# Optimization experiments

Hardware: AMD Instinct MI355X
Metric: run time of the kernel (lower is better)

The kernel has to match this reference:

```python
import jax, jax.numpy as jnp
import numpy as np

B, C, P, NG, NCLS, HID, N, IMG = 2, 256, 7, 2, 81, 1024, 512, 800
STRIDES = [4, 8, 16, 32]
SCALE = 56.0  # roi_map_level_scale


def _roi_align(feat, rois, pooled, scale, ng):
    """torchvision-legacy (aligned=False) ROI Align. feat [B,C,H,W], rois [N,5]."""
    Bf, Cf, H, W = feat.shape
    ft = jnp.transpose(feat, (0, 2, 3, 1))  # [B,H,W,C]
    b = rois[:, 0].astype(jnp.int32)
    x1, y1, x2, y2 = (rois[:, i] * scale for i in (1, 2, 3, 4))
    rw = jnp.maximum(x2 - x1, 1.0)
    rh = jnp.maximum(y2 - y1, 1.0)
    # sample grid per output bin: ng points per axis, centered in sub-bins
    g = (jnp.arange(pooled)[:, None] + (jnp.arange(ng)[None, :] + 0.5) / ng).reshape(-1)  # [P*ng]
    ys = y1[:, None] + g[None, :] * (rh / pooled)[:, None]  # [N,S]
    xs = x1[:, None] + g[None, :] * (rw / pooled)[:, None]

    def axis(coord, size):
        valid = (coord >= -1.0) & (coord <= size)
        c = jnp.clip(coord, 0.0, size - 1)
        lo = jnp.floor(c).astype(jnp.int32)
        hi = jnp.minimum(lo + 1, size - 1)
        return valid, lo, hi, c - lo

    vy, ylo, yhi, fy = axis(ys, H)
    vx, xlo, xhi, fx = axis(xs, W)
    bb = b[:, None, None]

    def gather(yi, xi):
        return ft[bb, yi[:, :, None], xi[:, None, :], :]  # [N,S,S,C]

    wy = fy[:, :, None, None]
    wx = fx[:, None, :, None]
    val = ((1 - wy) * (1 - wx) * gather(ylo, xlo) + (1 - wy) * wx * gather(ylo, xhi)
           + wy * (1 - wx) * gather(yhi, xlo) + wy * wx * gather(yhi, xhi))
    val = jnp.where((vy[:, :, None] & vx[:, None, :])[..., None], val, 0.0)
    val = val.reshape(-1, pooled, ng, pooled, ng, Cf).mean(axis=(2, 4))  # [N,P,P,C]
    return jnp.transpose(val, (0, 3, 1, 2))  # [N,C,P,P]


def setup_inputs() -> dict:
    key = jax.random.key(0)
    ks = jax.random.split(key, 16)
    feats = {}
    for i, s in enumerate(STRIDES):
        hw = IMG // s
        feats[f"p{i+2}"] = jax.random.normal(ks[i], (B, C, hw, hw), jnp.float32)
    # realistic proposals: batch idx + boxes with sizes 16..512 px
    bidx = jax.random.randint(ks[4], (N,), 0, B).astype(jnp.float32)
    sw = 2.0 ** jax.random.uniform(ks[5], (N,), minval=4.0, maxval=9.0)
    sh = 2.0 ** jax.random.uniform(ks[6], (N,), minval=4.0, maxval=9.0)
    x1 = jax.random.uniform(ks[7], (N,)) * (IMG - sw)
    y1 = jax.random.uniform(ks[8], (N,)) * (IMG - sh)
    rois = jnp.stack([bidx, x1, y1, x1 + sw - 1, y1 + sh - 1], axis=1)
    D = C * P * P
    inp = dict(feats, rois=rois,
               w1=0.01 * jax.random.normal(ks[9], (HID, D), jnp.float32),
               b1=jnp.zeros((HID,), jnp.float32),
               w2=0.01 * jax.random.normal(ks[10], (HID, HID), jnp.float32),
               b2=jnp.zeros((HID,), jnp.float32),
               w_cls=0.01 * jax.random.normal(ks[11], (NCLS, HID), jnp.float32),
               b_cls=jnp.zeros((NCLS,), jnp.float32),
               w_reg=0.001 * jax.random.normal(ks[12], (NCLS * 4, HID), jnp.float32),
               b_reg=jnp.zeros((NCLS * 4,), jnp.float32))
    return inp


def reference(p2, p3, p4, p5, rois, w1, b1, w2, b2, w_cls, b_cls, w_reg, b_reg):
    feats = [p2, p3, p4, p5]
    # FPN level assignment (same math as torch: log2(sqrt(hw)/scale + 1e-6), floor, clamp)
    rh = rois[:, 4] - rois[:, 2] + 1
    rw = rois[:, 3] - rois[:, 1] + 1
    levels = jnp.clip(jnp.floor(jnp.log2(jnp.sqrt(rh * rw) / SCALE + 1e-6)), 0, 3).astype(jnp.int32)
    # dispatch: compute each ROI on its assigned level (masked combine == gather/sort-scatter)
    pooled = jnp.zeros((rois.shape[0], C, P, P), rois.dtype)
    for l, feat in enumerate(feats):
        pl = _roi_align(feat, rois, P, 1.0 / STRIDES[l], NG)
        pooled = pooled + jnp.where((levels == l)[:, None, None, None], pl, 0.0)
    x = pooled.reshape(pooled.shape[0], -1)  # [N, C*P*P]
    x = jax.nn.relu(x @ w1.T + b1)
    x = jax.nn.relu(x @ w2.T + b2)
    x_cls = x @ w_cls.T + b_cls
    x_reg = x @ w_reg.T + b_reg  # TEST mode, not class-agnostic: no gather
    cls_probs = jax.nn.softmax(x_cls, axis=1)
    rois_out = rois.reshape(B, -1, 5)
    cls_probs = cls_probs.reshape(B, rois_out.shape[1], -1)
    bbox_preds = x_reg.reshape(B, rois_out.shape[1], -1)
    return rois_out, cls_probs, bbox_preds
```

## Files before the change

### kernel.cpp

```cpp
#include <hip/hip_runtime.h>
#include <hip/hip_bf16.h>
#include <math.h>

#define NROI   512
#define CCH    256
#define POOLP  7
#define DDIM   12544
#define HIDN   1024
#define NCLS   81
#define NREG   324
#define NHEAD  512
#define OUT_ROIS   2560
#define OUT_CLS    (512*81)

typedef __attribute__((ext_vector_type(4))) float f32x4;
typedef __attribute__((ext_vector_type(8))) short bf16x8;

static __device__ __forceinline__ unsigned short f2bf(float x) {
    __hip_bfloat16 h = __float2bfloat16(x);
    return *reinterpret_cast<unsigned short*>(&h);
}
static __device__ __forceinline__ float bf2f(unsigned short u) {
    unsigned int b = ((unsigned int)u) << 16;
    return *reinterpret_cast<float*>(&b);
}

#define PS_B0 10
#define PS_B1 (PS_B0 + 768)
#define PS_B2 (PS_B1 + 1024)
#define PS_B3 (PS_B2 + 1024)
__global__ __launch_bounds__(256) void prep_small_k(const float* __restrict__ rois,
                                                    const float* __restrict__ w2,
                                                    const float* __restrict__ wc,
                                                    const float* __restrict__ wr,
                                                    float* __restrict__ out,
                                                    float* __restrict__ accz,
                                                    unsigned short* __restrict__ w2b,
                                                    unsigned short* __restrict__ whd) {
    int bid = blockIdx.x, t = threadIdx.x;
    if (bid < PS_B0) {
        int i = bid * 256 + t;
        if (i < OUT_ROIS) out[i] = rois[i];
    } else if (bid < PS_B1) {
        int i = (bid - PS_B0) * 256 + t;
        ((float4*)accz)[i] = make_float4(0.f, 0.f, 0.f, 0.f);
    } else if (bid < PS_B2) {
        int i = (bid - PS_B1) * 256 + t;
        float4 v = ((const float4*)w2)[i];
        ushort4 o;
        o.x = f2bf(v.x); o.y = f2bf(v.y); o.z = f2bf(v.z); o.w = f2bf(v.w);
        ((ushort4*)w2b)[i] = o;
    } else {
        int i2 = (bid - PS_B2) * 256 + t;
        int r = i2 >> 9, c = (i2 & 511) << 1;
        float v0, v1;
        if (r < NCLS)             { v0 = wc[r * HIDN + c]; v1 = wc[r * HIDN + c + 1]; }
        else if (r < NCLS + NREG) { v0 = wr[(r - NCLS) * HIDN + c]; v1 = wr[(r - NCLS) * HIDN + c + 1]; }
        else                      { v0 = 0.f; v1 = 0.f; }
        ((unsigned int*)whd)[i2] = (unsigned int)f2bf(v0) | ((unsigned int)f2bf(v1) << 16);
    }
}

__global__ __launch_bounds__(256) void permute_w1_k(const float* __restrict__ w1,
                                                    unsigned short* __restrict__ w1b) {
    __shared__ unsigned short lw[49 * 258];
    int n = blockIdx.x, t = threadIdx.x;
    const float* src = w1 + (size_t)n * DDIM;
    for (int k = t; k < DDIM; k += 256) {
        int c = k / 49;
        int s = k - c * 49;
        lw[s * 258 + c] = f2bf(src[k]);
    }
    __syncthreads();
    unsigned int* dst = (unsigned int*)(w1b + (size_t)n * DDIM);
    for (int j2 = t; j2 < DDIM / 2; j2 += 256) {
        int s = j2 >> 7, c2 = (j2 & 127) << 1;
        dst[j2] = lw[s * 258 + c2] | ((unsigned int)lw[s * 258 + c2 + 1] << 16);
    }
}

__global__ __launch_bounds__(256) void transpose_k(const float* __restrict__ p2,
                                                   const float* __restrict__ p3,
                                                   const float* __restrict__ p4,
                                                   const float* __restrict__ p5,
                                                   unsigned short* __restrict__ f0,
                                                   unsigned short* __restrict__ f1,
                                                   unsigned short* __restrict__ f2,
                                                   unsigned short* __restrict__ f3) {
    __shared__ unsigned short sm[64][264];
    int idx = blockIdx.x;
    const float* in; unsigned short* op; int S, nS, base;
    if (idx < 1250)      { in = p2; op = f0; S = 40000; nS = 625; base = 0; }
    else if (idx < 1564) { in = p3; op = f1; S = 10000; nS = 157; base = 1250; }
    else if (idx < 1644) { in = p4; op = f2; S = 2500;  nS = 40;  base = 1564; }
    else                 { in = p5; op = f3; S = 625;   nS = 10;  base = 1644; }
    int j  = idx - base;
    int b  = j / nS;
    int s0 = (j - b * nS) * 64;
    int t  = threadIdx.x;

    int k = t & 15, g = t >> 4;
    bool vec = (s0 + 64 <= S);
    const float* src0 = in + ((size_t)(b * CCH + g * 16)) * S + s0 + k * 4;
#pragma unroll
    for (int jj = 0; jj < 16; jj++) {
        const float* src = src0 + (size_t)jj * S;
        int c = g * 16 + jj;
        if (vec) {
            float4 v = *(const float4*)src;
            sm[k * 4 + 0][c] = f2bf(v.x); sm[k * 4 + 1][c] = f2bf(v.y);
            sm[k * 4 + 2][c] = f2bf(v.z); sm[k * 4 + 3][c] = f2bf(v.w);
        } else {
#pragma unroll
            for (int e = 0; e < 4; e++)
                sm[k * 4 + e][c] = (s0 + k * 4 + e < S) ? f2bf(src[e]) : (unsigned short)0;
        }
    }
    __syncthreads();

    int L = t & 63, w = t >> 6;
#pragma unroll
    for (int i = 0; i < 16; i++) {
        int s = w * 16 + i;
        if (s0 + s < S) {
            ushort4 u = *(const ushort4*)&sm[s][4 * L];
            uint2 v;
            v.x = (unsigned int)u.x | ((unsigned int)u.y << 16);
            v.y = (unsigned int)u.z | ((unsigned int)u.w << 16);
            *(uint2*)(op + ((size_t)b * S + s0 + s) * CCH + 4 * L) = v;
        }
    }
}

__global__ __launch_bounds__(256) void roi_align_k(const unsigned short* __restrict__ f0,
                                                   const unsigned short* __restrict__ f1,
                                                   const unsigned short* __restrict__ f2,
                                                   const unsigned short* __restrict__ f3,
                                                   const float* __restrict__ rois,
                                                   unsigned short* __restrict__ xpool) {
    __shared__ float s_f[16];
    __shared__ int   s_lo[16], s_hi[16], s_v[16];

    int py = blockIdx.x, r = blockIdx.y, t = threadIdx.x;

    float r0  = rois[r * 5 + 0];
    float rx1 = rois[r * 5 + 1], ry1 = rois[r * 5 + 2];
    float rx2 = rois[r * 5 + 3], ry2 = rois[r * 5 + 4];
    int b = (int)r0;

    float aw = rx2 - rx1 + 1.f, ah = ry2 - ry1 + 1.f;
    float lvf = floorf(log2f(sqrtf(ah * aw) / 56.f + 1e-6f));
    int lv = (int)fminf(fmaxf(lvf, 0.f), 3.f);

    const unsigned short* F = (lv == 0) ? f0 : (lv == 1) ? f1 : (lv == 2) ? f2 : f3;
    int HW      = (lv == 0) ? 200 : (lv == 1) ? 100 : (lv == 2) ? 50 : 25;
    float scale = (lv == 0) ? 0.25f : (lv == 1) ? 0.125f : (lv == 2) ? 0.0625f : 0.03125f;

    float x1 = rx1 * scale, yy1 = ry1 * scale;
    float x2 = rx2 * scale, yy2 = ry2 * scale;
    float rw = fmaxf(x2 - x1, 1.f), rh = fmaxf(yy2 - yy1, 1.f);

    if (t < 16) {
        bool isY = t < 2;
        float coord;
        if (isY) {
            float g = (float)py + ((float)t + 0.5f) * 0.5f;
            coord = yy1 + g * (rh * (1.f / 7.f));
        } else {
            int j = t - 2;
            float g = (float)(j >> 1) + ((float)(j & 1) + 0.5f) * 0.5f;
            coord = x1 + g * (rw * (1.f / 7.f));
        }
        int vld = (coord >= -1.f && coord <= (float)HW) ? 1 : 0;
        float c = fminf(fmaxf(coord, 0.f), (float)(HW - 1));
        int lo  = (int)floorf(c);
        int hi  = min(lo + 1, HW - 1);
        s_v[t] = vld; s_lo[t] = lo; s_hi[t] = hi; s_f[t] = c - (float)lo;
    }
    __syncthreads();

    const unsigned short* Fb = F + ((size_t)b * HW * HW) * CCH + t;
    size_t obase = (size_t)r * DDIM + py * 7 * 256 + t;

    for (int px = 0; px < POOLP; px++) {
        float acc = 0.f;
#pragma unroll
        for (int s = 0; s < 4; s++) {
            int iy = s >> 1;
            int ix = px * 2 + (s & 1);
            int vy = s_v[iy], vx = s_v[2 + ix];
            if (vy & vx) {
                float fy = s_f[iy], fx = s_f[2 + ix];
                int ylo = s_lo[iy], yhi = s_hi[iy];
                int xlo = s_lo[2 + ix], xhi = s_hi[2 + ix];
                float v00 = bf2f(Fb[((size_t)ylo * HW + xlo) * CCH]);
                float v01 = bf2f(Fb[((size_t)ylo * HW + xhi) * CCH]);
                float v10 = bf2f(Fb[((size_t)yhi * HW + xlo) * CCH]);
                float v11 = bf2f(Fb[((size_t)yhi * HW + xhi) * CCH]);
                acc += (1.f - fy) * ((1.f - fx) * v00 + fx * v01)
                     + fy * ((1.f - fx) * v10 + fx * v11);
            }
        }
        xpool[obase + px * 256] = f2bf(acc * 0.25f);
    }
}

__global__ __launch_bounds__(256) void roi_align_nchw_k(const float* __restrict__ f0,
                                                        const float* __restrict__ f1,
                                                        const float* __restrict__ f2,
                                                        const float* __restrict__ f3,
                                                        const float* __restrict__ rois,
                                                        unsigned short* __restrict__ xpool) {
    __shared__ float s_f[16];
    __shared__ int   s_lo[16], s_hi[16], s_v[16];
    int py = blockIdx.x, r = blockIdx.y, t = threadIdx.x;
    float r0  = rois[r * 5 + 0];
    float rx1 = rois[r * 5 + 1], ry1 = rois[r * 5 + 2];
    float rx2 = rois[r * 5 + 3], ry2 = rois[r * 5 + 4];
    int b = (int)r0;
    float aw = rx2 - rx1 + 1.f, ah = ry2 - ry1 + 1.f;
    float lvf = floorf(log2f(sqrtf(ah * aw) / 56.f + 1e-6f));
    int lv = (int)fminf(fmaxf(lvf, 0.f), 3.f);
    const float* F = (lv == 0) ? f0 : (lv == 1) ? f1 : (lv == 2) ? f2 : f3;
    int HW      = (lv == 0) ? 200 : (lv == 1) ? 100 : (lv == 2) ? 50 : 25;
    float scale = (lv == 0) ? 0.25f : (lv == 1) ? 0.125f : (lv == 2) ? 0.0625f : 0.03125f;
    float x1 = rx1 * scale, yy1 = ry1 * scale;
    float x2 = rx2 * scale, yy2 = ry2 * scale;
    float rw = fmaxf(x2 - x1, 1.f), rh = fmaxf(yy2 - yy1, 1.f);
    if (t < 16) {
        bool isY = t < 2;
        float coord;
        if (isY) {
            float g = (float)py + ((float)t + 0.5f) * 0.5f;
            coord = yy1 + g * (rh * (1.f / 7.f));
        } else {
            int j = t - 2;
            float g = (float)(j >> 1) + ((float)(j & 1) + 0.5f) * 0.5f;
            coord = x1 + g * (rw * (1.f / 7.f));
        }
        int vld = (coord >= -1.f && coord <= (float)HW) ? 1 : 0;
        float c = fminf(fmaxf(coord, 0.f), (float)(HW - 1));
        int lo  = (int)floorf(c);
        int hi  = min(lo + 1, HW - 1);
        s_v[t] = vld; s_lo[t] = lo; s_hi[t] = hi; s_f[t] = c - (float)lo;
    }
    __syncthreads();
    const float* Fb = F + ((size_t)b * CCH + t) * HW * HW;
    size_t obase = (size_t)r * DDIM + py * 7 * 256 + t;
    for (int px = 0; px < POOLP; px++) {
        float acc = 0.f;
#pragma unroll
        for (int s = 0; s < 4; s++) {
            int iy = s >> 1, ix = px * 2 + (s & 1);
            int vy = s_v[iy], vx = s_v[2 + ix];
            if (vy & vx) {
                float fy = s_f[iy], fx = s_f[2 + ix];
                int ylo = s_lo[iy], yhi = s_hi[iy];
                int xlo = s_lo[2 + ix], xhi = s_hi[2 + ix];
                float v00 = Fb[(size_t)ylo * HW + xlo];
                float v01 = Fb[(size_t)ylo * HW + xhi];
                float v10 = Fb[(size_t)yhi * HW + xlo];
                float v11 = Fb[(size_t)yhi * HW + xhi];
                acc += (1.f - fy) * ((1.f - fx) * v00 + fx * v01)
                     + fy * ((1.f - fx) * v10 + fx * v11);
            }
        }
        xpool[obase + px * 256] = f2bf(acc * 0.25f);
    }
}

__global__ __launch_bounds__(256) void gemm_bf16_k(const unsigned short* __restrict__ A,
                                                   const unsigned short* __restrict__ W,
                                                   float* __restrict__ Cacc,
                                                   int M, int N, int K, int kchunk) {
    __shared__ __align__(16) unsigned short As[2][8][64][8];
    __shared__ __align__(16) unsigned short Ws[2][8][64][8];

    int t = threadIdx.x;
    int lane = t & 63, wid = t >> 6;
    int m0 = blockIdx.y * 64, n0 = blockIdx.x * 64;
    int k0 = blockIdx.z * kchunk;
    int wm = (wid >> 1) * 32, wn = (wid & 1) * 32;
    int fr = lane & 15, kg = lane >> 4;
    int nsteps = kchunk >> 6;

    f32x4 acc[2][2] = {};

    const unsigned short* Arow = A + (size_t)(m0 + lane) * K;
    const unsigned short* Wrow = W + (size_t)(n0 + lane) * K;

    auto stage = [&](int buf, int kb) {
#pragma unroll
        for (int i = 0; i < 2; i++) {
            int c = wid * 2 + i;
            __builtin_amdgcn_global_load_lds(
                (const __attribute__((address_space(1))) void*)(Arow + kb + c * 8),
                (__attribute__((address_space(3))) void*)(&As[buf][c][0][0]), 16, 0, 0);
            __builtin_amdgcn_global_load_lds(
                (const __attribute__((address_space(1))) void*)(Wrow + kb + c * 8),
                (__attribute__((address_space(3))) void*)(&Ws[buf][c][0][0]), 16, 0, 0);
        }
    };

    stage(0, k0);
    __syncthreads();
    int cur = 0;
    for (int tt = 0; tt < nsteps; ++tt) {
        if (tt + 1 < nsteps) stage(cur ^ 1, k0 + (tt + 1) * 64);
#pragma unroll
        for (int h = 0; h < 2; h++) {
            bf16x8 a0 = *(const bf16x8*)(&As[cur][h * 4 + kg][wm + fr][0]);
            bf16x8 a1 = *(const bf16x8*)(&As[cur][h * 4 + kg][wm + 16 + fr][0]);
            bf16x8 b0 = *(const bf16x8*)(&Ws[cur][h * 4 + kg][wn + fr][0]);
            bf16x8 b1 = *(const bf16x8*)(&Ws[cur][h * 4 + kg][wn + 16 + fr][0]);
            acc[0][0] = __builtin_amdgcn_mfma_f32_16x16x32_bf16(a0, b0, acc[0][0], 0, 0, 0);
            acc[0][1] = __builtin_amdgcn_mfma_f32_16x16x32_bf16(a0, b1, acc[0][1], 0, 0, 0);
            acc[1][0] = __builtin_amdgcn_mfma_f32_16x16x32_bf16(a1, b0, acc[1][0], 0, 0, 0);
            acc[1][1] = __builtin_amdgcn_mfma_f32_16x16x32_bf16(a1, b1, acc[1][1], 0, 0, 0);
        }
        __syncthreads();
        cur ^= 1;
    }

    int row = m0 + wm + (lane >> 4) * 4;
    int col = n0 + wn + fr;
#pragma unroll
    for (int fm = 0; fm < 2; fm++)
#pragma unroll
        for (int fn = 0; fn < 2; fn++)
#pragma unroll
            for (int r = 0; r < 4; r++)
                atomicAdd(&Cacc[(size_t)(row + fm * 16 + r) * N + col + fn * 16],
                          acc[fm][fn][r]);
}

__global__ __launch_bounds__(256) void gemm128_bf16_k(const unsigned short* __restrict__ A,
                                                      const unsigned short* __restrict__ W,
                                                      float* __restrict__ Cp,
                                                      int M, int N, int K, int kchunk) {
    __shared__ __align__(16) unsigned short As[2][8][64][8];
    __shared__ __align__(16) unsigned short Ws[2][8][128][8];

    int lin  = blockIdx.x;
    int nb   = (lin & 7) * 112 + (lin >> 3);
    int tile = nb / 14, bz = nb - tile * 14;
    int bx = tile >> 3, by = tile & 7;

    int t = threadIdx.x;
    int lane = t & 63, wid = t >> 6;
    int m0 = by * 64, n0 = bx * 128;
    int k0 = bz * kchunk;
    int wm = (wid >> 1) * 32, wn = (wid & 1) * 64;
    int fr = lane & 15, kg = lane >> 4;
    int nsteps = kchunk >> 6;

    f32x4 acc[2][4] = {};

    const unsigned short* Arow = A + (size_t)(m0 + lane) * K;

    auto stage = [&](int buf, int kb) {
#pragma unroll
        for (int i = 0; i < 6; i++) {
            int c = wid * 6 + i;
            if (c < 8) {
                __builtin_amdgcn_global_load_lds(
                    (const __attribute__((address_space(1))) void*)(Arow + kb + c * 8),
                    (__attribute__((address_space(3))) void*)(&As[buf][c][0][0]), 16, 0, 0);
            } else {
                int idx = c - 8, kgc = idx & 7, rh = idx >> 3;
                __builtin_amdgcn_global_load_lds(
                    (const __attribute__((address_space(1))) void*)
                        (W + (size_t)(n0 + rh * 64 + lane) * K + kb + kgc * 8),
                    (__attribute__((address_space(3))) void*)(&Ws[buf][kgc][rh * 64][0]),
                    16, 0, 0);
            }
        }
    };

    stage(0, k0);
    __syncthreads();
    int cur = 0;
    for (int tt = 0; tt < nsteps; ++tt) {
        if (tt + 1 < nsteps) stage(cur ^ 1, k0 + (tt + 1) * 64);
#pragma unroll
        for (int h = 0; h < 2; h++) {
            bf16x8 av[2], bv[4];
#pragma unroll
            for (int f = 0; f < 2; f++)
                av[f] = *(const bf16x8*)(&As[cur][h * 4 + kg][wm + f * 16 + fr][0]);
#pragma unroll
            for (int f = 0; f < 4; f++)
                bv[f] = *(const bf16x8*)(&Ws[cur][h * 4 + kg][wn + f * 16 + fr][0]);
#pragma unroll
            for (int fm = 0; fm < 2; fm++)
#pragma unroll
                for (int fn = 0; fn < 4; fn++)
                    acc[fm][fn] = __builtin_amdgcn_mfma_f32_16x16x32_bf16(
                        av[fm], bv[fn], acc[fm][fn], 0, 0, 0);
        }
        __syncthreads();
        cur ^= 1;
    }

    float* Cout = Cp + (size_t)bz * ((size_t)M * N);
    int row = m0 + wm + (lane >> 4) * 4;
    int col = n0 + wn + fr;
#pragma unroll
    for (int fm = 0; fm < 2; fm++)
#pragma unroll
        for (int fn = 0; fn < 4; fn++)
#pragma unroll
            for (int r = 0; r < 4; r++)
                Cout[(size_t)(row + fm * 16 + r) * N + col + fn * 16] = acc[fm][fn][r];
}

__global__ __launch_bounds__(256) void fc_ep_k(const float* __restrict__ Cp,
                                               const float* __restrict__ bias,
                                               unsigned short* __restrict__ dst,
                                               int MN, int ks) {
    int i = blockIdx.x * 256 + threadIdx.x;
    if (i >= MN) return;
    float s = 0.f;
    for (int p = 0; p < ks; p++) s += Cp[(size_t)p * MN + i];
    s = fmaxf(s + bias[i & (HIDN - 1)], 0.f);
    dst[i] = f2bf(s);
}

__global__ void head_ep_k(const float* __restrict__ hf,
                          const float* __restrict__ bc,
                          const float* __restrict__ br,
                          float* __restrict__ out) {
    int r = blockIdx.x, l = threadIdx.x;
    const float* row = hf + (size_t)r * NHEAD;

    float* reg = out + OUT_ROIS + OUT_CLS + (size_t)r * NREG;
    for (int j = l; j < NREG; j += 64) reg[j] = row[NCLS + j] + br[j];

    float v0 = row[l] + bc[l];
    float v1 = (l + 64 < NCLS) ? row[l + 64] + bc[l + 64] : -INFINITY;
    float m = fmaxf(v0, v1);
#pragma unroll
    for (int o = 32; o; o >>= 1) m = fmaxf(m, __shfl_xor(m, o));
    float e0 = __expf(v0 - m);
    float e1 = (l + 64 < NCLS) ? __expf(v1 - m) : 0.f;
    float s = e0 + e1;
#pragma unroll
    for (int o = 32; o; o >>= 1) s += __shfl_xor(s, o);
    float inv = 1.f / s;
    float* cls = out + OUT_ROIS + (size_t)r * NCLS;
    cls[l] = e0 * inv;
    if (l + 64 < NCLS) cls[l + 64] = e1 * inv;
}

extern "C" void kernel_launch(void* const* d_in, const int* in_sizes, int n_in,
                              void* d_out, int out_size, void* d_ws, size_t ws_size,
                              hipStream_t stream) {
    const float* p2   = (const float*)d_in[0];
    const float* p3   = (const float*)d_in[1];
    const float* p4   = (const float*)d_in[2];
    const float* p5   = (const float*)d_in[3];
    const float* rois = (const float*)d_in[4];
    const float* w1   = (const float*)d_in[5];
    const float* b1   = (const float*)d_in[6];
    const float* w2   = (const float*)d_in[7];
    const float* b2   = (const float*)d_in[8];
    const float* wc   = (const float*)d_in[9];
    const float* bc   = (const float*)d_in[10];
    const float* wr   = (const float*)d_in[11];
    const float* br   = (const float*)d_in[12];

    float* out = (float*)d_out;

    const int KS1 = 14;

    char* p = (char*)d_ws;
    auto alloc = [&](size_t bytes) { char* r = p; p += (bytes + 255) & ~(size_t)255; return r; };
    unsigned short* xpool = (unsigned short*)alloc((size_t)NROI * DDIM * 2);
    unsigned short* y1b   = (unsigned short*)alloc((size_t)NROI * HIDN * 2);
    unsigned short* y2b   = (unsigned short*)alloc((size_t)NROI * HIDN * 2);
    unsigned short* w1b   = (unsigned short*)alloc((size_t)HIDN * DDIM * 2);
    unsigned short* w2b   = (unsigned short*)alloc((size_t)HIDN * HIDN * 2);
    unsigned short* whd   = (unsigned short*)alloc((size_t)NHEAD * HIDN * 2);
    float*          accz  = (float*)alloc((size_t)(NROI * HIDN + NROI * NHEAD) * 4);
    unsigned short* ft0 = (unsigned short*)alloc((size_t)2 * 40000 * CCH * 2);
    unsigned short* ft1 = (unsigned short*)alloc((size_t)2 * 10000 * CCH * 2);
    unsigned short* ft2 = (unsigned short*)alloc((size_t)2 * 2500 * CCH * 2);
    unsigned short* ft3 = (unsigned short*)alloc((size_t)2 * 625 * CCH * 2);
    bool nhwc = (size_t)(p - (char*)d_ws) <= ws_size;

    float* y2f = accz;
    float* hf  = accz + (size_t)NROI * HIDN;
    float* part = (float*)ft0;

    prep_small_k<<<PS_B3, 256, 0, stream>>>(rois, w2, wc, wr, out, accz, w2b, whd);
    permute_w1_k<<<HIDN, 256, 0, stream>>>(w1, w1b);

    if (nhwc) {
        transpose_k<<<1664, 256, 0, stream>>>(p2, p3, p4, p5, ft0, ft1, ft2, ft3);
        roi_align_k<<<dim3(POOLP, NROI), 256, 0, stream>>>(ft0, ft1, ft2, ft3, rois, xpool);
    } else {
        roi_align_nchw_k<<<dim3(POOLP, NROI), 256, 0, stream>>>(p2, p3, p4, p5, rois, xpool);
    }

    gemm128_bf16_k<<<8 * 8 * KS1, 256, 0, stream>>>(
        xpool, w1b, part, NROI, HIDN, DDIM, DDIM / KS1);
    fc_ep_k<<<(NROI * HIDN + 255) / 256, 256, 0, stream>>>(part, b1, y1b, NROI * HIDN, KS1);

    gemm_bf16_k<<<dim3(HIDN / 64, NROI / 64, 2), 256, 0, stream>>>(
        y1b, w2b, y2f, NROI, HIDN, HIDN, HIDN / 2);
    fc_ep_k<<<(NROI * HIDN + 255) / 256, 256, 0, stream>>>(y2f, b2, y2b, NROI * HIDN, 1);

    gemm_bf16_k<<<dim3(NHEAD / 64, NROI / 64, 4), 256, 0, stream>>>(
        y2b, whd, hf, NROI, NHEAD, HIDN, HIDN / 4);
    head_ep_k<<<NROI, 64, 0, stream>>>(hf, bc, br, out);
}
```

Measured before the change: 185.1 us.

## Merge weight prep kernels, retile feature transpose, fuse FC2 epilogue into GEMM

Three changes at once. The w1 permute is folded into the small prep kernel, removing one launch. The NCHW-to-NHWC transpose now uses 128-spatial by 64-channel tiles with an XOR-swizzled LDS layout in place of padding. The second FC GEMM drops its split-K atomics, the zeroing of its accumulator and the separate epilogue kernel, and applies bias plus ReLU directly while writing bf16. The cost is that FC2 now runs on only 128 blocks with no K split, which lowers parallelism, and the transpose's LDS reads become scalar 2-byte accesses.

```diff
diff --git a/kernel.cpp b/kernel.cpp
--- a/kernel.cpp
+++ b/kernel.cpp
@@ -26,31 +26,35 @@
 }
 
 #define PS_B0 10
-#define PS_B1 (PS_B0 + 768)
+#define PS_B1 (PS_B0 + 256)
 #define PS_B2 (PS_B1 + 1024)
 #define PS_B3 (PS_B2 + 1024)
-__global__ __launch_bounds__(256) void prep_small_k(const float* __restrict__ rois,
-                                                    const float* __restrict__ w2,
-                                                    const float* __restrict__ wc,
-                                                    const float* __restrict__ wr,
-                                                    float* __restrict__ out,
-                                                    float* __restrict__ accz,
-                                                    unsigned short* __restrict__ w2b,
-                                                    unsigned short* __restrict__ whd) {
+#define PS_B4 (PS_B3 + 1024)
+__global__ __launch_bounds__(256) void prep_k(const float* __restrict__ rois,
+                                              const float* __restrict__ w1,
+                                              const float* __restrict__ w2,
+                                              const float* __restrict__ wc,
+                                              const float* __restrict__ wr,
+                                              float* __restrict__ out,
+                                              float* __restrict__ hf,
+                                              unsigned short* __restrict__ w1b,
+                                              unsigned short* __restrict__ w2b,
+                                              unsigned short* __restrict__ whd) {
+    __shared__ unsigned short lw[49 * 258];
     int bid = blockIdx.x, t = threadIdx.x;
     if (bid < PS_B0) {
         int i = bid * 256 + t;
         if (i < OUT_ROIS) out[i] = rois[i];
     } else if (bid < PS_B1) {
         int i = (bid - PS_B0) * 256 + t;
-        ((float4*)accz)[i] = make_float4(0.f, 0.f, 0.f, 0.f);
+        ((float4*)hf)[i] = make_float4(0.f, 0.f, 0.f, 0.f);
     } else if (bid < PS_B2) {
         int i = (bid - PS_B1) * 256 + t;
         float4 v = ((const float4*)w2)[i];
         ushort4 o;
         o.x = f2bf(v.x); o.y = f2bf(v.y); o.z = f2bf(v.z); o.w = f2bf(v.w);
         ((ushort4*)w2b)[i] = o;
-    } else {
+    } else if (bid < PS_B3) {
         int i2 = (bid - PS_B2) * 256 + t;
         int r = i2 >> 9, c = (i2 & 511) << 1;
         float v0, v1;
@@ -58,24 +62,20 @@
         else if (r < NCLS + NREG) { v0 = wr[(r - NCLS) * HIDN + c]; v1 = wr[(r - NCLS) * HIDN + c + 1]; }
         else                      { v0 = 0.f; v1 = 0.f; }
         ((unsigned int*)whd)[i2] = (unsigned int)f2bf(v0) | ((unsigned int)f2bf(v1) << 16);
-    }
-}
-
-__global__ __launch_bounds__(256) void permute_w1_k(const float* __restrict__ w1,
-                                                    unsigned short* __restrict__ w1b) {
-    __shared__ unsigned short lw[49 * 258];
-    int n = blockIdx.x, t = threadIdx.x;
-    const float* src = w1 + (size_t)n * DDIM;
-    for (int k = t; k < DDIM; k += 256) {
-        int c = k / 49;
-        int s = k - c * 49;
-        lw[s * 258 + c] = f2bf(src[k]);
-    }
-    __syncthreads();
-    unsigned int* dst = (unsigned int*)(w1b + (size_t)n * DDIM);
-    for (int j2 = t; j2 < DDIM / 2; j2 += 256) {
-        int s = j2 >> 7, c2 = (j2 & 127) << 1;
-        dst[j2] = lw[s * 258 + c2] | ((unsigned int)lw[s * 258 + c2 + 1] << 16);
+    } else {
+        int n = bid - PS_B3;
+        const float* src = w1 + (size_t)n * DDIM;
+        for (int k = t; k < DDIM; k += 256) {
+            int c = k / 49;
+            int s = k - c * 49;
+            lw[s * 258 + c] = f2bf(src[k]);
+        }
+        __syncthreads();
+        unsigned int* dst = (unsigned int*)(w1b + (size_t)n * DDIM);
+        for (int j2 = t; j2 < DDIM / 2; j2 += 256) {
+            int s = j2 >> 7, c2 = (j2 & 127) << 1;
+            dst[j2] = lw[s * 258 + c2] | ((unsigned int)lw[s * 258 + c2 + 1] << 16);
+        }
     }
 }
 
@@ -87,47 +87,58 @@
                                                    unsigned short* __restrict__ f1,
                                                    unsigned short* __restrict__ f2,
                                                    unsigned short* __restrict__ f3) {
-    __shared__ unsigned short sm[64][264];
+    __shared__ unsigned short sm[128][66];
     int idx = blockIdx.x;
-    const float* in; unsigned short* op; int S, nS, base;
-    if (idx < 1250)      { in = p2; op = f0; S = 40000; nS = 625; base = 0; }
-    else if (idx < 1564) { in = p3; op = f1; S = 10000; nS = 157; base = 1250; }
-    else if (idx < 1644) { in = p4; op = f2; S = 2500;  nS = 40;  base = 1564; }
-    else                 { in = p5; op = f3; S = 625;   nS = 10;  base = 1644; }
-    int j  = idx - base;
-    int b  = j / nS;
-    int s0 = (j - b * nS) * 64;
+    const float* in; unsigned short* op; int S, base;
+    if (idx < 313)      { in = p2; op = f0; S = 40000; base = 0; }
+    else if (idx < 392) { in = p3; op = f1; S = 10000; base = 313; }
+    else if (idx < 412) { in = p4; op = f2; S = 2500;  base = 392; }
+    else                { in = p5; op = f3; S = 625;   base = 412; }
+    int s0 = (idx - base) * 128;
+    int c0 = blockIdx.y * 64;
+    int b  = blockIdx.z;
     int t  = threadIdx.x;
 
-    int k = t & 15, g = t >> 4;
-    bool vec = (s0 + 64 <= S);
-    const float* src0 = in + ((size_t)(b * CCH + g * 16)) * S + s0 + k * 4;
-#pragma unroll
-    for (int jj = 0; jj < 16; jj++) {
-        const float* src = src0 + (size_t)jj * S;
-        int c = g * 16 + jj;
+    int k = t & 31, g = t >> 5;
+    bool vec = (s0 + 128 <= S);
+#pragma unroll
+    for (int jj = 0; jj < 8; jj++) {
+        int c = g + jj * 8;
+        const float* src = in + ((size_t)(b * CCH + c0 + c)) * S + s0 + k * 4;
         if (vec) {
             float4 v = *(const float4*)src;
-            sm[k * 4 + 0][c] = f2bf(v.x); sm[k * 4 + 1][c] = f2bf(v.y);
-            sm[k * 4 + 2][c] = f2bf(v.z); sm[k * 4 + 3][c] = f2bf(v.w);
+#pragma unroll
+            for (int e = 0; e < 4; e++) {
+                int s = k * 4 + e;
+                float val = (e == 0) ? v.x : (e == 1) ? v.y : (e == 2) ? v.z : v.w;
+                sm[s][c ^ ((s & 7) << 3)] = f2bf(val);
+            }
         } else {
 #pragma unroll
-            for (int e = 0; e < 4; e++)
-                sm[k * 4 + e][c] = (s0 + k * 4 + e < S) ? f2bf(src[e]) : (unsigned short)0;
+            for (int e = 0; e < 4; e++) {
+                int s = k * 4 + e;
+                sm[s][c ^ ((s & 7) << 3)] =
+                    (s0 + s < S) ? f2bf(src[e]) : (unsigned short)0;
+            }
         }
     }
     __syncthreads();
 
-    int L = t & 63, w = t >> 6;
-#pragma unroll
-    for (int i = 0; i < 16; i++) {
-        int s = w * 16 + i;
+    int lane = t & 63, w = t >> 6;
+    int rl = lane >> 4, cw = (lane & 15) * 4;
+#pragma unroll
+    for (int i = 0; i < 8; i++) {
+        int s = w * 32 + i * 4 + rl;
         if (s0 + s < S) {
-            ushort4 u = *(const ushort4*)&sm[s][4 * L];
+            int sw = (s & 7) << 3;
+            unsigned short u0 = sm[s][(cw + 0) ^ sw];
+            unsigned short u1 = sm[s][(cw + 1) ^ sw];
+            unsigned short u2 = sm[s][(cw + 2) ^ sw];
+            unsigned short u3 = sm[s][(cw + 3) ^ sw];
             uint2 v;
-            v.x = (unsigned int)u.x | ((unsigned int)u.y << 16);
-            v.y = (unsigned int)u.z | ((unsigned int)u.w << 16);
-            *(uint2*)(op + ((size_t)b * S + s0 + s) * CCH + 4 * L) = v;
+            v.x = (unsigned int)u0 | ((unsigned int)u1 << 16);
+            v.y = (unsigned int)u2 | ((unsigned int)u3 << 16);
+            *(uint2*)(op + ((size_t)b * S + s0 + s) * CCH + c0 + cw) = v;
         }
     }
 }
@@ -334,6 +345,74 @@
                           acc[fm][fn][r]);
 }
 
+__global__ __launch_bounds__(256) void gemm_fc2_k(const unsigned short* __restrict__ A,
+                                                  const unsigned short* __restrict__ W,
+                                                  const float* __restrict__ bias,
+                                                  unsigned short* __restrict__ dst,
+                                                  int M, int N, int K) {
+    __shared__ __align__(16) unsigned short As[2][8][64][8];
+    __shared__ __align__(16) unsigned short Ws[2][8][64][8];
+
+    int t = threadIdx.x;
+    int lane = t & 63, wid = t >> 6;
+    int m0 = blockIdx.y * 64, n0 = blockIdx.x * 64;
+    int wm = (wid >> 1) * 32, wn = (wid & 1) * 32;
+    int fr = lane & 15, kg = lane >> 4;
+    int nsteps = K >> 6;
+
+    f32x4 acc[2][2] = {};
+
+    const unsigned short* Arow = A + (size_t)(m0 + lane) * K;
+    const unsigned short* Wrow = W + (size_t)(n0 + lane) * K;
+
+    auto stage = [&](int buf, int kb) {
+#pragma unroll
+        for (int i = 0; i < 2; i++) {
+            int c = wid * 2 + i;
+            __builtin_amdgcn_global_load_lds(
+                (const __attribute__((address_space(1))) void*)(Arow + kb + c * 8),
+                (__attribute__((address_space(3))) void*)(&As[buf][c][0][0]), 16, 0, 0);
+            __builtin_amdgcn_global_load_lds(
+                (const __attribute__((address_space(1))) void*)(Wrow + kb + c * 8),
+                (__attribute__((address_space(3))) void*)(&Ws[buf][c][0][0]), 16, 0, 0);
+        }
+    };
+
+    stage(0, 0);
+    __syncthreads();
+    int cur = 0;
+    for (int tt = 0; tt < nsteps; ++tt) {
+        if (tt + 1 < nsteps) stage(cur ^ 1, (tt + 1) * 64);
+#pragma unroll
+        for (int h = 0; h < 2; h++) {
+            bf16x8 a0 = *(const bf16x8*)(&As[cur][h * 4 + kg][wm + fr][0]);
+            bf16x8 a1 = *(const bf16x8*)(&As[cur][h * 4 + kg][wm + 16 + fr][0]);
+            bf16x8 b0 = *(const bf16x8*)(&Ws[cur][h * 4 + kg][wn + fr][0]);
+            bf16x8 b1 = *(const bf16x8*)(&Ws[cur][h * 4 + kg][wn + 16 + fr][0]);
+            acc[0][0] = __builtin_amdgcn_mfma_f32_16x16x32_bf16(a0, b0, acc[0][0], 0, 0, 0);
+            acc[0][1] = __builtin_amdgcn_mfma_f32_16x16x32_bf16(a0, b1, acc[0][1], 0, 0, 0);
+            acc[1][0] = __builtin_amdgcn_mfma_f32_16x16x32_bf16(a1, b0, acc[1][0], 0, 0, 0);
+            acc[1][1] = __builtin_amdgcn_mfma_f32_16x16x32_bf16(a1, b1, acc[1][1], 0, 0, 0);
+        }
+        __syncthreads();
+        cur ^= 1;
+    }
+
+    int row = m0 + wm + (lane >> 4) * 4;
+    int col = n0 + wn + fr;
+#pragma unroll
+    for (int fm = 0; fm < 2; fm++)
+#pragma unroll
+        for (int fn = 0; fn < 2; fn++) {
+            float bv = bias[col + fn * 16];
+#pragma unroll
+            for (int r = 0; r < 4; r++) {
+                float v = fmaxf(acc[fm][fn][r] + bv, 0.f);
+                dst[(size_t)(row + fm * 16 + r) * N + col + fn * 16] = f2bf(v);
+            }
+        }
+}
+
 __global__ __launch_bounds__(256) void gemm128_bf16_k(const unsigned short* __restrict__ A,
                                                       const unsigned short* __restrict__ W,
                                                       float* __restrict__ Cp,
@@ -481,22 +560,20 @@
     unsigned short* w1b   = (unsigned short*)alloc((size_t)HIDN * DDIM * 2);
     unsigned short* w2b   = (unsigned short*)alloc((size_t)HIDN * HIDN * 2);
     unsigned short* whd   = (unsigned short*)alloc((size_t)NHEAD * HIDN * 2);
-    float*          accz  = (float*)alloc((size_t)(NROI * HIDN + NROI * NHEAD) * 4);
+    float*          hf    = (float*)alloc((size_t)NROI * NHEAD * 4);
     unsigned short* ft0 = (unsigned short*)alloc((size_t)2 * 40000 * CCH * 2);
     unsigned short* ft1 = (unsigned short*)alloc((size_t)2 * 10000 * CCH * 2);
     unsigned short* ft2 = (unsigned short*)alloc((size_t)2 * 2500 * CCH * 2);
     unsigned short* ft3 = (unsigned short*)alloc((size_t)2 * 625 * CCH * 2);
     bool nhwc = (size_t)(p - (char*)d_ws) <= ws_size;
 
-    float* y2f = accz;
-    float* hf  = accz + (size_t)NROI * HIDN;
     float* part = (float*)ft0;
 
-    prep_small_k<<<PS_B3, 256, 0, stream>>>(rois, w2, wc, wr, out, accz, w2b, whd);
-    permute_w1_k<<<HIDN, 256, 0, stream>>>(w1, w1b);
+    prep_k<<<PS_B4, 256, 0, stream>>>(rois, w1, w2, wc, wr, out, hf, w1b, w2b, whd);
 
     if (nhwc) {
-        transpose_k<<<1664, 256, 0, stream>>>(p2, p3, p4, p5, ft0, ft1, ft2, ft3);
+        transpose_k<<<dim3(417, 4, 2), 256, 0, stream>>>(p2, p3, p4, p5,
+                                                         ft0, ft1, ft2, ft3);
         roi_align_k<<<dim3(POOLP, NROI), 256, 0, stream>>>(ft0, ft1, ft2, ft3, rois, xpool);
     } else {
         roi_align_nchw_k<<<dim3(POOLP, NROI), 256, 0, stream>>>(p2, p3, p4, p5, rois, xpool);
@@ -506,9 +583,8 @@
         xpool, w1b, part, NROI, HIDN, DDIM, DDIM / KS1);
     fc_ep_k<<<(NROI * HIDN + 255) / 256, 256, 0, stream>>>(part, b1, y1b, NROI * HIDN, KS1);
 
-    gemm_bf16_k<<<dim3(HIDN / 64, NROI / 64, 2), 256, 0, stream>>>(
-        y1b, w2b, y2f, NROI, HIDN, HIDN, HIDN / 2);
-    fc_ep_k<<<(NROI * HIDN + 255) / 256, 256, 0, stream>>>(y2f, b2, y2b, NROI * HIDN, 1);
+    gemm_fc2_k<<<dim3(HIDN / 64, NROI / 64), 256, 0, stream>>>(
+        y1b, w2b, b2, y2b, NROI, HIDN, HIDN);
 
     gemm_bf16_k<<<dim3(NHEAD / 64, NROI / 64, 4), 256, 0, stream>>>(
         y2b, whd, hf, NROI, NHEAD, HIDN, HIDN / 4);
```

New measurement: 180.5 us. -2.5%, faster.
